# Performance work log

Measured on AMD Instinct MI355X. Metric: run time of the kernel, lower is better.

The kernel has to match this reference:

```python
import jax, jax.numpy as jnp
import numpy as np

DIM = 128
HEADS = 8
DIM_HEAD = 16
INNER = DIM * DIM_HEAD  # 2048, per source: inner_dim = dim * dim_head
SCALE = DIM ** (-0.5)   # per source: scale = dim ** -0.5


def setup_inputs() -> dict:
    key = jax.random.key(0)
    k1, k2, k3, k4, k5 = jax.random.split(key, 5)
    tensor = jax.random.normal(k1, (4, 4, 1024, DIM), dtype=jnp.float32)
    latents = jax.random.normal(k2, (4, 4, 64, DIM), dtype=jnp.float32)
    # Linear(dim, inner_dim, bias=False) etc.; stored as [in, out] for x @ W
    Wq = jax.random.normal(k3, (DIM, INNER), dtype=jnp.float32) * (DIM ** -0.5)
    Wkv = jax.random.normal(k4, (DIM, 2 * INNER), dtype=jnp.float32) * (DIM ** -0.5)
    Wo = jax.random.normal(k5, (INNER, DIM), dtype=jnp.float32) * (INNER ** -0.5)
    return {"tensor": tensor, "latents": latents, "Wq": Wq, "Wkv": Wkv, "Wo": Wo}


def _split_heads(x):
    # b t n (h d) -> b h t n d
    b, t, n, hd = x.shape
    d = hd // HEADS
    return x.reshape(b, t, n, HEADS, d).transpose(0, 3, 1, 2, 4)


def reference(tensor, latents, Wq, Wkv, Wo):
    q = latents @ Wq                                  # [b,t,nl,inner]
    kv_input = jnp.concatenate((tensor, latents), axis=-2)  # [b,t,nm+nl,dim]
    kv = kv_input @ Wkv
    k, v = jnp.split(kv, 2, axis=-1)
    q, k, v = map(_split_heads, (q, k, v))            # [b,h,t,n,d]
    q = q * SCALE
    sim = jnp.einsum('bhtid,bhtjd->bhtij', q, k)
    attn = jax.nn.softmax(sim, axis=-1)               # stable softmax (matches max-subtraction)
    out = jnp.einsum('bhtij,bhtjd->bhtid', attn, v)
    # b h t n d -> b t n (h d)
    b, h, t, n, d = out.shape
    out = out.transpose(0, 2, 3, 1, 4).reshape(b, t, n, h * d)
    return out @ Wo
```

## Files before the change

kernel.cpp:

```cpp
#include <hip/hip_runtime.h>

typedef __bf16 bf16x8 __attribute__((ext_vector_type(8)));
typedef __bf16 bf16x4 __attribute__((ext_vector_type(4)));
typedef float  f32x4  __attribute__((ext_vector_type(4)));

#define SCALE2 (0.08838834764831845f * 1.4426950408889634f)
#define M0 64.0f

__device__ __forceinline__ f32x4 mfma16(bf16x8 a, bf16x8 b, f32x4 c) {
  return __builtin_amdgcn_mfma_f32_16x16x32_bf16(a, b, c, 0, 0, 0);
}

__global__ __launch_bounds__(256, 1) void pa_pre(
    const float* __restrict__ Wq, const float* __restrict__ Wkv,
    const float* __restrict__ Wo, __bf16* __restrict__ Mt,
    __bf16* __restrict__ Nt) {
  const int g = blockIdx.x;
  const int mn = g >> 7, h = (g >> 4) & 7, rch = g & 15;
  const int R = rch * 8;
  const int tid = threadIdx.x;
  const int hc = h * 256;
  __shared__ float As[128][260];
  __shared__ float Bv[8][260];

  if (mn == 0) {
    for (int i = tid; i < 8 * 64; i += 256) {
      const int b = i >> 6, c4 = (i & 63) * 4;
      *(float4*)&Bv[b][c4] = *(const float4*)&Wkv[(size_t)(R + b) * 4096 + hc + c4];
    }
  } else {
    for (int i = tid; i < 512; i += 256) {
      const int c = i >> 1, q = (i & 1) * 4;
      const float4 v = *(const float4*)&Wo[(size_t)(hc + c) * 128 + R + q];
      Bv[q][c] = v.x; Bv[q + 1][c] = v.y; Bv[q + 2][c] = v.z; Bv[q + 3][c] = v.w;
    }
  }
  const float* abase = (mn == 0) ? (Wq + hc) : (Wkv + 2048 + hc);
  const size_t astride = (mn == 0) ? 2048 : 4096;
  for (int i = tid; i < 128 * 64; i += 256) {
    const int a = i >> 6, c4 = (i & 63) * 4;
    *(float4*)&As[a][c4] = *(const float4*)&abase[(size_t)a * astride + c4];
  }
  __syncthreads();

  const int a  = tid & 127;
  const int bh = (tid >> 7) * 4;
  float acc[4] = {0.f, 0.f, 0.f, 0.f};
  for (int c4 = 0; c4 < 256; c4 += 4) {
    const float4 av = *(const float4*)&As[a][c4];
    #pragma unroll
    for (int j = 0; j < 4; ++j) {
      const float4 bv = *(const float4*)&Bv[bh + j][c4];
      acc[j] += av.x * bv.x + av.y * bv.y + av.z * bv.z + av.w * bv.w;
    }
  }
  __bf16* dsth = (mn == 0 ? Mt : Nt) + (size_t)h * 16384;
  __bf16* dstl = dsth + (size_t)8 * 16384;
  const float sc = (mn == 0) ? SCALE2 : 1.0f;
  #pragma unroll
  for (int j = 0; j < 4; ++j) {
    const float v = acc[j] * sc;
    const __bf16 hi = (__bf16)v;
    dsth[(size_t)(R + bh + j) * 128 + a] = hi;
    dstl[(size_t)(R + bh + j) * 128 + a] = (__bf16)(v - (float)hi);
  }
}

__device__ __forceinline__ void stage_load(const float* __restrict__ src, int tid,
                                           float4 (&r)[4]) {
  const float4* s4 = (const float4*)(src + (size_t)(tid >> 3) * 128 + ((tid & 7) << 4));
  r[0] = s4[0]; r[1] = s4[1]; r[2] = s4[2]; r[3] = s4[3];
}
__device__ __forceinline__ void stage_write(const float4 (&r)[4], __bf16 (*dst)[152],
                                            int tid) {
  const int row = tid >> 3, colb = (tid & 7) << 4;
  bf16x8 lo, hi;
  lo[0] = (__bf16)r[0].x; lo[1] = (__bf16)r[0].y; lo[2] = (__bf16)r[0].z; lo[3] = (__bf16)r[0].w;
  lo[4] = (__bf16)r[1].x; lo[5] = (__bf16)r[1].y; lo[6] = (__bf16)r[1].z; lo[7] = (__bf16)r[1].w;
  hi[0] = (__bf16)r[2].x; hi[1] = (__bf16)r[2].y; hi[2] = (__bf16)r[2].z; hi[3] = (__bf16)r[2].w;
  hi[4] = (__bf16)r[3].x; hi[5] = (__bf16)r[3].y; hi[6] = (__bf16)r[3].z; hi[7] = (__bf16)r[3].w;
  *(bf16x8*)&dst[row][colb]     = lo;
  *(bf16x8*)&dst[row][colb + 8] = hi;
}

__global__ __launch_bounds__(512, 1) void pa_fused(
    const float* __restrict__ tensor,
    const float* __restrict__ latents,
    const __bf16* __restrict__ Mt,
    __bf16* __restrict__ Opart,
    float* __restrict__ Lpart)
{
  __shared__ __align__(16) __bf16 Xs[2][64][152];
  __shared__ __align__(16) __bf16 As[2][64][136];
  __shared__ __align__(16) __bf16 Xts[2][128][76];
  __shared__ __align__(16) __bf16 Ps[8][16][40];

  const int bid = blockIdx.x;
  const int bt  = bid >> 4;
  const int h   = (bid >> 1) & 7;
  const int js  = bid & 1;

  const int tid  = threadIdx.x;
  const int wave = tid >> 6;
  const int lane = tid & 63;
  const int l15  = lane & 15;
  const int lg   = lane >> 4;
  const int it   = wave >> 1;
  const int jsub = wave & 1;

  const float* latBT = latents + (size_t)bt * (64 * 128);
  const float* tenBT = tensor  + (size_t)bt * (1024 * 128);
  const int NT = js ? 8 : 9;

  auto xsrc = [&](int t) -> const float* {
    return js ? (tenBT + (size_t)(8 + t) * (64 * 128))
              : (t == 0 ? latBT : tenBT + (size_t)(t - 1) * (64 * 128));
  };

  bf16x8 ident;
  #pragma unroll
  for (int r = 0; r < 8; ++r)
    ident[r] = (lg * 8 + r == l15) ? (__bf16)1.0f : (__bf16)0.0f;

  for (int i = tid; i < 2 * 64 * 24; i += 512) {
    const int b = i / 1536, rem = i - b * 1536;
    Xs[b][rem / 24][128 + rem % 24] = (__bf16)0.0f;
  }
  {
    float4 st[4];
    stage_load(latBT, tid, st);
    stage_write(st, Xs[0], tid);
  }
  __syncthreads();

  {
    bf16x8 mh[4], ml[4];
    const __bf16* MtH = Mt + (size_t)h * 16384;
    const __bf16* MtL = MtH + (size_t)8 * 16384;
    #pragma unroll
    for (int kb = 0; kb < 4; ++kb) {
      mh[kb] = *(const bf16x8*)&MtH[(size_t)(wave * 16 + l15) * 128 + kb * 32 + lg * 8];
      ml[kb] = *(const bf16x8*)&MtL[(size_t)(wave * 16 + l15) * 128 + kb * 32 + lg * 8];
    }
    f32x4 accA[4] = {};
    #pragma unroll
    for (int kb = 0; kb < 4; ++kb)
      #pragma unroll
      for (int mt = 0; mt < 4; ++mt) {
        bf16x8 af = *(const bf16x8*)&Xs[0][mt * 16 + l15][kb * 32 + lg * 8];
        accA[mt] = mfma16(af, mh[kb], accA[mt]);
        accA[mt] = mfma16(af, ml[kb], accA[mt]);
      }
    #pragma unroll
    for (int mt = 0; mt < 4; ++mt)
      #pragma unroll
      for (int r = 0; r < 4; ++r) {
        const float v = accA[mt][r];
        const __bf16 hi = (__bf16)v;
        As[0][mt * 16 + lg * 4 + r][wave * 16 + l15] = hi;
        As[1][mt * 16 + lg * 4 + r][wave * 16 + l15] = (__bf16)(v - (float)hi);
      }
  }
  __syncthreads();

  bf16x8 qh[4], ql[4];
  #pragma unroll
  for (int kb = 0; kb < 4; ++kb) {
    qh[kb] = *(const bf16x8*)&As[0][it * 16 + l15][kb * 32 + lg * 8];
    ql[kb] = *(const bf16x8*)&As[1][it * 16 + l15][kb * 32 + lg * 8];
  }
  {
    float4 st[4];
    if (js) stage_load(xsrc(0), tid, st);
    if (js) stage_write(st, Xs[0], tid);
  }
  __syncthreads();

  float lrow[4] = {0.f, 0.f, 0.f, 0.f};
  f32x4 oacc[8] = {};

  for (int t = 0; t < NT; ++t) {
    const int cb = t & 1, nb = cb ^ 1;
    const bool pf = (t + 1 < NT);
    float4 st[4];
    if (pf) stage_load(xsrc(t + 1), tid, st);

    if (t > 0) {
      bf16x8 pfr = *(const bf16x8*)&Ps[wave][l15][lg * 8];
      #pragma unroll
      for (int dt = 0; dt < 8; ++dt) {
        bf16x8 vb = *(const bf16x8*)&Xts[nb][dt * 16 + l15][jsub * 32 + lg * 8];
        oacc[dt] = mfma16(pfr, vb, oacc[dt]);
      }
    }

    f32x4 sacc[2] = {};
    #pragma unroll
    for (int kb = 0; kb < 4; ++kb)
      #pragma unroll
      for (int jt = 0; jt < 2; ++jt) {
        bf16x8 kf = *(const bf16x8*)&Xs[cb][jsub * 32 + jt * 16 + l15][kb * 32 + lg * 8];
        sacc[jt] = mfma16(qh[kb], kf, sacc[jt]);
        sacc[jt] = mfma16(ql[kb], kf, sacc[jt]);
      }

    #pragma unroll
    for (int r = 0; r < 4; ++r) {
      const float p0 = exp2f(sacc[0][r] - M0);
      const float p1 = exp2f(sacc[1][r] - M0);
      sacc[0][r] = p0; sacc[1][r] = p1;
      lrow[r] += p0 + p1;
    }

    #pragma unroll
    for (int jt = 0; jt < 2; ++jt)
      #pragma unroll
      for (int r = 0; r < 4; ++r)
        Ps[wave][lg * 4 + r][jt * 16 + l15] = (__bf16)sacc[jt][r];

    #pragma unroll
    for (int ds = 0; ds < 4; ++ds) {
      const int dbase = ((wave & 1) * 4 + ds) * 16;
      bf16x8 at = *(const bf16x8*)&Xs[cb][(wave >> 1) * 16 + l15][dbase + lg * 8];
      f32x4 tp = mfma16(at, ident, (f32x4){0.f, 0.f, 0.f, 0.f});
      bf16x4 tb;
      tb[0] = (__bf16)tp[0]; tb[1] = (__bf16)tp[1];
      tb[2] = (__bf16)tp[2]; tb[3] = (__bf16)tp[3];
      *(bf16x4*)&Xts[cb][dbase + l15][(wave >> 1) * 16 + lg * 4] = tb;
    }

    if (pf) stage_write(st, Xs[nb], tid);
    __syncthreads();
  }

  {
    bf16x8 pfr = *(const bf16x8*)&Ps[wave][l15][lg * 8];
    #pragma unroll
    for (int dt = 0; dt < 8; ++dt) {
      bf16x8 vb = *(const bf16x8*)&Xts[(NT - 1) & 1][dt * 16 + l15][jsub * 32 + lg * 8];
      oacc[dt] = mfma16(pfr, vb, oacc[dt]);
    }
  }

  #pragma unroll
  for (int r = 0; r < 4; ++r) {
    float s = lrow[r];
    s += __shfl_xor(s, 1);
    s += __shfl_xor(s, 2);
    s += __shfl_xor(s, 4);
    s += __shfl_xor(s, 8);
    lrow[r] = s;
  }

  const int jsplit = js * 2 + jsub;
  const size_t ob = ((((size_t)jsplit * 16 + bt) * 8 + h) * 64) * 128;
  #pragma unroll
  for (int dt = 0; dt < 8; ++dt)
    #pragma unroll
    for (int r = 0; r < 4; ++r)
      Opart[ob + (size_t)(it * 16 + lg * 4 + r) * 128 + dt * 16 + l15] =
          (__bf16)oacc[dt][r];

  const size_t mb = (((size_t)jsplit * 16 + bt) * 8 + h) * 64;
  if (l15 == 0)
    #pragma unroll
    for (int r = 0; r < 4; ++r)
      Lpart[mb + it * 16 + lg * 4 + r] = lrow[r];
}

__global__ __launch_bounds__(256, 2) void pa_mproj(
    const __bf16* __restrict__ Opart, const float* __restrict__ Lpart,
    const __bf16* __restrict__ Nt, float* __restrict__ part)
{
  __shared__ float linvS[64];
  __shared__ __align__(16) __bf16 Bs[2][64][136];

  const int bid = blockIdx.x;
  const int bt = bid >> 4, h = (bid >> 1) & 7, ch = bid & 1;
  const int tid = threadIdx.x;

  if (tid < 64) {
    float l = 0.f;
    #pragma unroll
    for (int s = 0; s < 4; ++s)
      l += Lpart[(((size_t)s * 16 + bt) * 8 + h) * 64 + tid];
    linvS[tid] = 1.0f / l;
  }
  __syncthreads();

  #pragma unroll
  for (int k = 0; k < 4; ++k) {
    const int f = tid + k * 256;
    const int i = f >> 4, d8 = f & 15;
    float v[8] = {0.f, 0.f, 0.f, 0.f, 0.f, 0.f, 0.f, 0.f};
    #pragma unroll
    for (int s = 0; s < 4; ++s) {
      bf16x8 o8 = *(const bf16x8*)&Opart[(((size_t)s * 16 + bt) * 8 + h) * 8192 +
                                         (size_t)i * 128 + d8 * 8];
      #pragma unroll
      for (int e = 0; e < 8; ++e) v[e] += (float)o8[e];
    }
    const float inv = linvS[i];
    bf16x8 h8, l8;
    #pragma unroll
    for (int e = 0; e < 8; ++e) {
      const float x = v[e] * inv;
      h8[e] = (__bf16)x;
      l8[e] = (__bf16)(x - (float)h8[e]);
    }
    *(bf16x8*)&Bs[0][i][d8 * 8] = h8;
    *(bf16x8*)&Bs[1][i][d8 * 8] = l8;
  }
  __syncthreads();

  const int wave = tid >> 6, lane = tid & 63;
  const int l15 = lane & 15, lg = lane >> 4;
  const int ncol = ch * 64 + wave * 16 + l15;
  const __bf16* NtH = Nt + (size_t)h * 16384;
  const __bf16* NtL = NtH + (size_t)8 * 16384;
  bf16x8 nh[4], nl[4];
  #pragma unroll
  for (int kb = 0; kb < 4; ++kb) {
    nh[kb] = *(const bf16x8*)&NtH[(size_t)ncol * 128 + kb * 32 + lg * 8];
    nl[kb] = *(const bf16x8*)&NtL[(size_t)ncol * 128 + kb * 32 + lg * 8];
  }
  f32x4 acc[4] = {};
  #pragma unroll
  for (int kb = 0; kb < 4; ++kb)
    #pragma unroll
    for (int mt = 0; mt < 4; ++mt) {
      bf16x8 ah = *(const bf16x8*)&Bs[0][mt * 16 + l15][kb * 32 + lg * 8];
      bf16x8 al = *(const bf16x8*)&Bs[1][mt * 16 + l15][kb * 32 + lg * 8];
      acc[mt] = mfma16(ah, nh[kb], acc[mt]);
      acc[mt] = mfma16(al, nh[kb], acc[mt]);
      acc[mt] = mfma16(ah, nl[kb], acc[mt]);
    }
  const size_t pb = ((size_t)h * 16 + bt) * 8192;
  #pragma unroll
  for (int mt = 0; mt < 4; ++mt)
    #pragma unroll
    for (int r = 0; r < 4; ++r)
      part[pb + (size_t)(mt * 16 + lg * 4 + r) * 128 + ncol] = acc[mt][r];
}

__global__ __launch_bounds__(256) void pa_reduce(const float* __restrict__ part,
                                                 float* __restrict__ out) {
  const int idx = blockIdx.x * 256 + threadIdx.x;
  const f32x4* p4 = (const f32x4*)part;
  f32x4 s = p4[idx];
  #pragma unroll
  for (int g = 1; g < 8; ++g) s += p4[(size_t)g * 32768 + idx];
  ((f32x4*)out)[idx] = s;
}

extern "C" void kernel_launch(void* const* d_in, const int* in_sizes, int n_in,
                              void* d_out, int out_size, void* d_ws, size_t ws_size,
                              hipStream_t stream) {
  const float* tensor  = (const float*)d_in[0];
  const float* latents = (const float*)d_in[1];
  const float* Wq      = (const float*)d_in[2];
  const float* Wkv     = (const float*)d_in[3];
  const float* Wo      = (const float*)d_in[4];
  float* out = (float*)d_out;

  __bf16* Mt    = (__bf16*)d_ws;
  __bf16* Nt    = Mt + (size_t)2 * 8 * 128 * 128;
  __bf16* Opart = Nt + (size_t)2 * 8 * 128 * 128;
  float*  Lpart = (float*)(Opart + (size_t)4 * 16 * 8 * 64 * 128);
  float*  part  = Lpart + (size_t)4 * 16 * 8 * 64;

  pa_pre<<<256, 256, 0, stream>>>(Wq, Wkv, Wo, Mt, Nt);
  pa_fused<<<256, 512, 0, stream>>>(tensor, latents, Mt, Opart, Lpart);
  pa_mproj<<<256, 256, 0, stream>>>(Opart, Lpart, Nt, part);
  pa_reduce<<<128, 256, 0, stream>>>(part, out);
}
```

Baseline: 107.2 us.

## Split fused attention KV range four ways and shrink shared memory for occupancy

The fused attention kernel now splits each (batch-time, head) key range into four chunks instead of two, launching 512 blocks rather than 256, and the merge kernel sums eight partials instead of four. Shared memory is cut by removing row padding, aliasing the As buffer onto Xts, and dropping the zero-fill loop, and launch bounds now allow four blocks per CU. The score MFMAs use separate hi/lo accumulators to break the dependency chain, and the transpose loads skip unused lanes. In exchange, the partial-output traffic doubles and the reduction does more work, and the smaller padding may add LDS bank conflicts.

```diff
diff --git a/kernel.cpp b/kernel.cpp
--- a/kernel.cpp
+++ b/kernel.cpp
@@ -71,7 +71,7 @@
   const float4* s4 = (const float4*)(src + (size_t)(tid >> 3) * 128 + ((tid & 7) << 4));
   r[0] = s4[0]; r[1] = s4[1]; r[2] = s4[2]; r[3] = s4[3];
 }
-__device__ __forceinline__ void stage_write(const float4 (&r)[4], __bf16 (*dst)[152],
+__device__ __forceinline__ void stage_write(const float4 (&r)[4], __bf16 (*dst)[136],
                                             int tid) {
   const int row = tid >> 3, colb = (tid & 7) << 4;
   bf16x8 lo, hi;
@@ -83,22 +83,22 @@
   *(bf16x8*)&dst[row][colb + 8] = hi;
 }
 
-__global__ __launch_bounds__(512, 1) void pa_fused(
+__global__ __launch_bounds__(512, 4) void pa_fused(
     const float* __restrict__ tensor,
     const float* __restrict__ latents,
     const __bf16* __restrict__ Mt,
     __bf16* __restrict__ Opart,
     float* __restrict__ Lpart)
 {
-  __shared__ __align__(16) __bf16 Xs[2][64][152];
-  __shared__ __align__(16) __bf16 As[2][64][136];
-  __shared__ __align__(16) __bf16 Xts[2][128][76];
-  __shared__ __align__(16) __bf16 Ps[8][16][40];
+  __shared__ __align__(16) __bf16 Xs[2][64][136];
+  __shared__ __align__(16) __bf16 Xts[2][128][68];
+  __shared__ __align__(16) __bf16 Ps[8][16][36];
+  __bf16 (*As)[64][136] = reinterpret_cast<__bf16 (*)[64][136]>(&Xts[0][0][0]);
 
   const int bid = blockIdx.x;
-  const int bt  = bid >> 4;
-  const int h   = (bid >> 1) & 7;
-  const int js  = bid & 1;
+  const int bt  = bid >> 5;
+  const int h   = (bid >> 2) & 7;
+  const int js2 = bid & 3;
 
   const int tid  = threadIdx.x;
   const int wave = tid >> 6;
@@ -110,11 +110,11 @@
 
   const float* latBT = latents + (size_t)bt * (64 * 128);
   const float* tenBT = tensor  + (size_t)bt * (1024 * 128);
-  const int NT = js ? 8 : 9;
+  const int NT = (js2 == 0) ? 5 : 4;
 
   auto xsrc = [&](int t) -> const float* {
-    return js ? (tenBT + (size_t)(8 + t) * (64 * 128))
-              : (t == 0 ? latBT : tenBT + (size_t)(t - 1) * (64 * 128));
+    return (js2 == 0) ? (t == 0 ? latBT : tenBT + (size_t)(t - 1) * (64 * 128))
+                      : (tenBT + (size_t)(js2 * 4 + t) * (64 * 128));
   };
 
   bf16x8 ident;
@@ -122,10 +122,6 @@
   for (int r = 0; r < 8; ++r)
     ident[r] = (lg * 8 + r == l15) ? (__bf16)1.0f : (__bf16)0.0f;
 
-  for (int i = tid; i < 2 * 64 * 24; i += 512) {
-    const int b = i / 1536, rem = i - b * 1536;
-    Xs[b][rem / 24][128 + rem % 24] = (__bf16)0.0f;
-  }
   {
     float4 st[4];
     stage_load(latBT, tid, st);
@@ -171,8 +167,8 @@
   }
   {
     float4 st[4];
-    if (js) stage_load(xsrc(0), tid, st);
-    if (js) stage_write(st, Xs[0], tid);
+    if (js2) stage_load(xsrc(0), tid, st);
+    if (js2) stage_write(st, Xs[0], tid);
   }
   __syncthreads();
 
@@ -194,34 +190,36 @@
       }
     }
 
-    f32x4 sacc[2] = {};
+    f32x4 sh[2] = {}, sl[2] = {};
     #pragma unroll
     for (int kb = 0; kb < 4; ++kb)
       #pragma unroll
       for (int jt = 0; jt < 2; ++jt) {
         bf16x8 kf = *(const bf16x8*)&Xs[cb][jsub * 32 + jt * 16 + l15][kb * 32 + lg * 8];
-        sacc[jt] = mfma16(qh[kb], kf, sacc[jt]);
-        sacc[jt] = mfma16(ql[kb], kf, sacc[jt]);
+        sh[jt] = mfma16(qh[kb], kf, sh[jt]);
+        sl[jt] = mfma16(ql[kb], kf, sl[jt]);
       }
 
+    float p[2][4];
     #pragma unroll
     for (int r = 0; r < 4; ++r) {
-      const float p0 = exp2f(sacc[0][r] - M0);
-      const float p1 = exp2f(sacc[1][r] - M0);
-      sacc[0][r] = p0; sacc[1][r] = p1;
-      lrow[r] += p0 + p1;
+      p[0][r] = exp2f(sh[0][r] + sl[0][r] - M0);
+      p[1][r] = exp2f(sh[1][r] + sl[1][r] - M0);
+      lrow[r] += p[0][r] + p[1][r];
     }
 
     #pragma unroll
     for (int jt = 0; jt < 2; ++jt)
       #pragma unroll
       for (int r = 0; r < 4; ++r)
-        Ps[wave][lg * 4 + r][jt * 16 + l15] = (__bf16)sacc[jt][r];
+        Ps[wave][lg * 4 + r][jt * 16 + l15] = (__bf16)p[jt][r];
 
     #pragma unroll
     for (int ds = 0; ds < 4; ++ds) {
       const int dbase = ((wave & 1) * 4 + ds) * 16;
-      bf16x8 at = *(const bf16x8*)&Xs[cb][(wave >> 1) * 16 + l15][dbase + lg * 8];
+      bf16x8 at = {};
+      if (lg < 2)
+        at = *(const bf16x8*)&Xs[cb][(wave >> 1) * 16 + l15][dbase + lg * 8];
       f32x4 tp = mfma16(at, ident, (f32x4){0.f, 0.f, 0.f, 0.f});
       bf16x4 tb;
       tb[0] = (__bf16)tp[0]; tb[1] = (__bf16)tp[1];
@@ -252,7 +250,7 @@
     lrow[r] = s;
   }
 
-  const int jsplit = js * 2 + jsub;
+  const int jsplit = js2 * 2 + jsub;
   const size_t ob = ((((size_t)jsplit * 16 + bt) * 8 + h) * 64) * 128;
   #pragma unroll
   for (int dt = 0; dt < 8; ++dt)
@@ -282,7 +280,7 @@
   if (tid < 64) {
     float l = 0.f;
     #pragma unroll
-    for (int s = 0; s < 4; ++s)
+    for (int s = 0; s < 8; ++s)
       l += Lpart[(((size_t)s * 16 + bt) * 8 + h) * 64 + tid];
     linvS[tid] = 1.0f / l;
   }
@@ -294,7 +292,7 @@
     const int i = f >> 4, d8 = f & 15;
     float v[8] = {0.f, 0.f, 0.f, 0.f, 0.f, 0.f, 0.f, 0.f};
     #pragma unroll
-    for (int s = 0; s < 4; ++s) {
+    for (int s = 0; s < 8; ++s) {
       bf16x8 o8 = *(const bf16x8*)&Opart[(((size_t)s * 16 + bt) * 8 + h) * 8192 +
                                          (size_t)i * 128 + d8 * 8];
       #pragma unroll
@@ -366,11 +364,11 @@
   __bf16* Mt    = (__bf16*)d_ws;
   __bf16* Nt    = Mt + (size_t)2 * 8 * 128 * 128;
   __bf16* Opart = Nt + (size_t)2 * 8 * 128 * 128;
-  float*  Lpart = (float*)(Opart + (size_t)4 * 16 * 8 * 64 * 128);
-  float*  part  = Lpart + (size_t)4 * 16 * 8 * 64;
+  float*  Lpart = (float*)(Opart + (size_t)8 * 16 * 8 * 64 * 128);
+  float*  part  = Lpart + (size_t)8 * 16 * 8 * 64;
 
   pa_pre<<<256, 256, 0, stream>>>(Wq, Wkv, Wo, Mt, Nt);
-  pa_fused<<<256, 512, 0, stream>>>(tensor, latents, Mt, Opart, Lpart);
+  pa_fused<<<512, 512, 0, stream>>>(tensor, latents, Mt, Opart, Lpart);
   pa_mproj<<<256, 256, 0, stream>>>(Opart, Lpart, Nt, part);
   pa_reduce<<<128, 256, 0, stream>>>(part, out);
 }
```

Measured after the change: 114.6 us. +6.9%, slower.
